# Kernel optimization log

Measured on AMD Instinct MI355X. Metric: run time of the kernel, lower is better.

Reference implementation:

```python
import jax, jax.numpy as jnp
import numpy as np

H = 128          # num_hidden
B, L, K, M = 4, 2048, 24, 64   # batch, residues, neighbors-per-residue, ligand atoms
FF = 4 * H       # feed-forward width
EPS = 1e-5       # LayerNorm eps (torch default)


def _gelu(x):
    return jax.nn.gelu(x, approximate=False)  # torch nn.GELU default (erf)


def _ln(x, s, b):
    mu = jnp.mean(x, axis=-1, keepdims=True)
    var = jnp.mean(jnp.square(x - mu), axis=-1, keepdims=True)
    return (x - mu) * jax.lax.rsqrt(var + EPS) * s + b


def _lin(x, w, b):
    return x @ w.T + b


def setup_inputs() -> dict:
    key = jax.random.key(0)
    ks = iter(jax.random.split(key, 40))
    # uniqueness makes the reference deterministic and equal to scatter-add.
    nn_idx = jnp.argsort(jax.random.uniform(next(ks), (B, L, M)), axis=-1)[:, :, :K].astype(jnp.int32)
    inp = {
        "nn_idx": nn_idx,
        "Y_scale": jax.random.uniform(next(ks), (B, M), jnp.float32, 1.0, 30.0),
        "h_Y_nodes": jax.random.normal(next(ks), (B, L, K, H), jnp.float32),
        "h_E_context": jax.random.normal(next(ks), (B, L, K, H), jnp.float32),
        "h_V": jax.random.normal(next(ks), (B, L, H), jnp.float32),
    }
    def lin_params(fan_in, fan_out):
        w = jax.random.normal(next(ks), (fan_out, fan_in), jnp.float32) / np.sqrt(fan_in).astype(np.float32)
        b = jnp.zeros((fan_out,), jnp.float32)
        return w, b
    for name, fi, fo in [("W1", 3 * H, H), ("W2", H, H), ("W3", H, H),
                         ("W11", 3 * H, H), ("W12", H, H), ("W13", H, H),
                         ("Win", H, FF), ("Wout", FF, H)]:
        inp[name + "_w"], inp[name + "_b"] = lin_params(fi, fo)
    for name in ("n1", "n2", "n3"):
        inp[name + "_s"] = jnp.ones((H,), jnp.float32)
        inp[name + "_b"] = jnp.zeros((H,), jnp.float32)
    return inp


def reference(nn_idx, Y_scale, h_Y_nodes, h_E_context, h_V,
              W1_w, W1_b, W2_w, W2_b, W3_w, W3_b,
              W11_w, W11_b, W12_w, W12_b, W13_w, W13_b,
              Win_w, Win_b, Wout_w, Wout_b,
              n1_s, n1_b, n2_s, n2_b, n3_s, n3_b):
    h_V_exp = jnp.broadcast_to(h_V[:, :, None, :], (B, L, K, H))
    h_YEV = jnp.concatenate([h_Y_nodes, h_E_context, h_V_exp], axis=-1)  # [B,L,K,3H]
    msg = _lin(_gelu(_lin(_gelu(_lin(h_YEV, W1_w, W1_b)), W2_w, W2_b)), W3_w, W3_b)
    # scatter per (b,l) with unique idx, then sum over l == segment-sum over (b, atom)
    seg_ids = (jnp.arange(B, dtype=jnp.int32)[:, None, None] * M + nn_idx).reshape(-1)
    dh = jax.ops.segment_sum(msg.reshape(-1, H), seg_ids, num_segments=B * M).reshape(B, M, H)
    dh = dh / Y_scale[:, :, None]
    # gather_context_atom_features: dh[b, nn_idx[b,l,k]]
    dh = jnp.take_along_axis(dh, nn_idx.reshape(B, L * K)[:, :, None], axis=1).reshape(B, L, K, H)
    h_Y = _ln(h_Y_nodes + dh, n1_s, n1_b)
    h_Y = _ln(h_Y + _lin(_gelu(_lin(h_Y, Win_w, Win_b)), Wout_w, Wout_b), n2_s, n2_b)
    h_YEV = jnp.concatenate([h_Y, h_E_context, h_V_exp], axis=-1)
    msg = _lin(_gelu(_lin(_gelu(_lin(h_YEV, W11_w, W11_b)), W12_w, W12_b)), W13_w, W13_b)
    h_E = _ln(h_E_context + msg, n3_s, n3_b)
    return (h_Y, h_E)
```

## Files before the change

kernel.cpp:

```cpp
#include <hip/hip_runtime.h>
#include <hip/hip_bf16.h>

#define H_   128
#define B_   4
#define L_   2048
#define KN   24
#define M_   64
#define NROW (B_*L_*KN)
#define LKR  (L_*KN)

typedef float f32x4 __attribute__((ext_vector_type(4)));
typedef short s16x8 __attribute__((ext_vector_type(8)));

#define MFMA16(a,b,c) __builtin_amdgcn_mfma_f32_16x16x32_bf16((a),(b),(c),0,0,0)

static __device__ __forceinline__ unsigned short f2bfu(float x){
    union { __hip_bfloat16 h; unsigned short s; } u; u.h = __float2bfloat16(x); return u.s;
}
static __device__ __forceinline__ float bf2f(unsigned short s){
    union { unsigned short s; __hip_bfloat16 h; } u; u.s = s; return __bfloat162float(u.h);
}
static __device__ __forceinline__ unsigned packbf(float lo, float hi){
    return (unsigned)f2bfu(lo) | ((unsigned)f2bfu(hi) << 16);
}
static __device__ __forceinline__ float gelu_f(float x){
    const float x2 = x*x;
    const float u  = x * fmaf(x2, -0.10294265f, -2.3022083f);
    const float e  = __builtin_amdgcn_exp2f(u);
    return x * __builtin_amdgcn_rcpf(1.0f + e);
}
static __device__ __forceinline__ float wsum(float v){
#pragma unroll
    for (int m = 32; m; m >>= 1) v += __shfl_xor(v, m, 64);
    return v;
}
static __device__ __forceinline__ s16x8 cvt8(float4 p0, float4 p1){
    s16x8 v;
    v[0]=(short)f2bfu(p0.x); v[1]=(short)f2bfu(p0.y); v[2]=(short)f2bfu(p0.z); v[3]=(short)f2bfu(p0.w);
    v[4]=(short)f2bfu(p1.x); v[5]=(short)f2bfu(p1.y); v[6]=(short)f2bfu(p1.z); v[7]=(short)f2bfu(p1.w);
    return v;
}
template<int KW>
static __device__ __forceinline__ s16x8 afrag(const short* xs, int r, int blk){
    return *(const s16x8*)(xs + r*KW + ((blk ^ (r & 7)) << 3));
}
template<int KW>
static __device__ __forceinline__ void bstore(short* xs, int r, int c, unsigned v){
    *(unsigned*)(xs + r*KW + ((((c >> 3) ^ (r & 7))) << 3) + (c & 7)) = v;
}
static __device__ __forceinline__ int fidx(int r, int c){
    return r*128 + ((((c >> 2) ^ (r & 7))) << 2) + (c & 3);
}

struct PackArgs {
    const float* src[8];
    int K[8];
    int off[8];
};
#define PACK_TOTAL 294912
__global__ void k_init(PackArgs pa, short* __restrict__ dst, float* __restrict__ dh){
    const int gid = blockIdx.x*256 + threadIdx.x;
    if (gid < B_*M_*H_) dh[gid] = 0.0f;
    if (gid >= PACK_TOTAL) return;
    int w = 0;
#pragma unroll
    for (int i = 1; i < 8; ++i) if (gid >= pa.off[i]) w = i;
    const int e = gid - pa.off[w];
    const int K = pa.K[w];
    const int j = e & 7, lane = (e >> 3) & 63, tt = e >> 9;
    const int kt = K >> 5;
    const int tk = tt % kt, tn = tt / kt;
    const int row = tn*16 + (lane & 15);
    const int col = tk*32 + ((lane >> 4) << 3) + j;
    dst[gid] = (short)f2bfu(pa.src[w][(size_t)row*K + col]);
}

__global__ __launch_bounds__(512, 4) void k_msg(
    const float* __restrict__ hY, const float* __restrict__ hE, const float* __restrict__ hV,
    const int* __restrict__ nn,
    const short* __restrict__ W1p, const float* __restrict__ B1,
    const short* __restrict__ W2p, const float* __restrict__ B2,
    const short* __restrict__ W3p, const float* __restrict__ B3,
    float* __restrict__ dh)
{
    __shared__ __align__(16) char pool[65536];
    short* xs  = (short*)pool;
    short* tb2 = (short*)pool;
    short* tb1 = (short*)(pool + 49152);
    const int tid = threadIdx.x, lane = tid & 63, w = tid >> 6;
    const int cl = lane & 15, rq = lane >> 4;
    const int row0 = blockIdx.x * 64, b = row0 / LKR;

    for (int c = tid; c < 64*48; c += 512){
        const int rr = c/48, k = (c - rr*48) << 3, g = row0 + rr;
        const float* s = (k < 128) ? hY + (size_t)g*128 + k
                      : (k < 256) ? hE + (size_t)g*128 + (k-128)
                                  : hV + (size_t)(g/KN)*128 + (k-256);
        float4 p0 = ((const float4*)s)[0], p1 = ((const float4*)s)[1];
        *(s16x8*)(xs + rr*384 + ((((k>>3) ^ (rr&7))) << 3)) = cvt8(p0, p1);
    }
    __syncthreads();

    f32x4 acc[4];
#pragma unroll
    for (int rf = 0; rf < 4; ++rf)
#pragma unroll
        for (int j = 0; j < 4; ++j) acc[rf][j] = B1[w*16 + rq*4 + j];
    {
        const s16x8* W8 = (const s16x8*)W1p;
#pragma unroll
        for (int ks = 0; ks < 12; ++ks){
            const s16x8 wf = W8[(size_t)(w*12 + ks)*64 + lane];
            const int blk = ks*4 + rq;
#pragma unroll
            for (int rf = 0; rf < 4; ++rf){
                const s16x8 a = afrag<384>(xs, rf*16 + cl, blk);
                acc[rf] = MFMA16(wf, a, acc[rf]);
            }
        }
    }
#pragma unroll
    for (int rf = 0; rf < 4; ++rf){
        const int r = rf*16 + cl, cb = w*16 + rq*4;
        bstore<128>(tb1, r, cb,   packbf(gelu_f(acc[rf][0]), gelu_f(acc[rf][1])));
        bstore<128>(tb1, r, cb+2, packbf(gelu_f(acc[rf][2]), gelu_f(acc[rf][3])));
    }
    __syncthreads();

#pragma unroll
    for (int rf = 0; rf < 4; ++rf)
#pragma unroll
        for (int j = 0; j < 4; ++j) acc[rf][j] = B2[w*16 + rq*4 + j];
    {
        const s16x8* W8 = (const s16x8*)W2p;
#pragma unroll
        for (int ks = 0; ks < 4; ++ks){
            const s16x8 wf = W8[(size_t)(w*4 + ks)*64 + lane];
            const int blk = ks*4 + rq;
#pragma unroll
            for (int rf = 0; rf < 4; ++rf){
                const s16x8 a = afrag<128>(tb1, rf*16 + cl, blk);
                acc[rf] = MFMA16(wf, a, acc[rf]);
            }
        }
    }
#pragma unroll
    for (int rf = 0; rf < 4; ++rf){
        const int r = rf*16 + cl, cb = w*16 + rq*4;
        bstore<128>(tb2, r, cb,   packbf(gelu_f(acc[rf][0]), gelu_f(acc[rf][1])));
        bstore<128>(tb2, r, cb+2, packbf(gelu_f(acc[rf][2]), gelu_f(acc[rf][3])));
    }
    __syncthreads();

#pragma unroll
    for (int rf = 0; rf < 4; ++rf){
        const float bv = B3[w*16 + cl];
        acc[rf] = (f32x4){bv,bv,bv,bv};
    }
    {
        const s16x8* W8 = (const s16x8*)W3p;
#pragma unroll
        for (int ks = 0; ks < 4; ++ks){
            const s16x8 wf = W8[(size_t)(w*4 + ks)*64 + lane];
            const int blk = ks*4 + rq;
#pragma unroll
            for (int rf = 0; rf < 4; ++rf){
                const s16x8 a = afrag<128>(tb2, rf*16 + cl, blk);
                acc[rf] = MFMA16(a, wf, acc[rf]);
            }
        }
    }
#pragma unroll
    for (int rf = 0; rf < 4; ++rf){
        int mj[4];
#pragma unroll
        for (int j = 0; j < 4; ++j) mj[j] = nn[row0 + rf*16 + rq*4 + j];
        const int c = w*16 + cl;
#pragma unroll
        for (int j = 0; j < 4; ++j)
            __hip_atomic_fetch_add(dh + ((size_t)(b*M_ + mj[j]))*128 + c, acc[rf][j],
                                   __ATOMIC_RELAXED, __HIP_MEMORY_SCOPE_AGENT);
    }
}

__global__ __launch_bounds__(512, 4) void k_hy(
    const float* __restrict__ hY, const float* __restrict__ dh, const float* __restrict__ Ys,
    const int* __restrict__ nn,
    const short* __restrict__ Winp, const float* __restrict__ Bin,
    const short* __restrict__ Woutp, const float* __restrict__ Bout,
    const float* __restrict__ n1s, const float* __restrict__ n1b,
    const float* __restrict__ n2s, const float* __restrict__ n2b,
    float* __restrict__ outY)
{
    __shared__ __align__(16) char pool[49152];
    short* xb  = (short*)pool;
    short* ffc = (short*)(pool + 16384);
    float* tf  = (float*)(pool + 16384);
    const int tid = threadIdx.x, lane = tid & 63, w = tid >> 6;
    const int cl = lane & 15, rq = lane >> 4;
    const int row0 = blockIdx.x * 64, b = row0 / LKR;
    const s16x8* Wi8 = (const s16x8*)Winp;
    const s16x8* Wo8 = (const s16x8*)Woutp;

    for (int c = tid; c < 64*16; c += 512){
        const int rr = c >> 4, k = (c & 15) << 3, g = row0 + rr;
        const int m = nn[g];
        const float inv = 1.0f / Ys[b*M_ + m];
        const float* a = hY + (size_t)g*128 + k;
        const float* d = dh + ((size_t)(b*M_ + m))*128 + k;
        float4 a0 = ((const float4*)a)[0], a1 = ((const float4*)a)[1];
        float4 d0 = ((const float4*)d)[0], d1 = ((const float4*)d)[1];
        float4 r0 = {fmaf(d0.x,inv,a0.x), fmaf(d0.y,inv,a0.y), fmaf(d0.z,inv,a0.z), fmaf(d0.w,inv,a0.w)};
        float4 r1 = {fmaf(d1.x,inv,a1.x), fmaf(d1.y,inv,a1.y), fmaf(d1.z,inv,a1.z), fmaf(d1.w,inv,a1.w)};
        const int s = rr & 7, kb = k >> 2;
        *(float4*)&tf[rr*128 + ((kb ^ s) << 2)]     = r0;
        *(float4*)&tf[rr*128 + (((kb+1) ^ s) << 2)] = r1;
    }
    __syncthreads();

#pragma unroll
    for (int i = 0; i < 8; ++i){
        const int r = w*8 + i;
        const float v0 = tf[fidx(r, lane)], v1 = tf[fidx(r, lane+64)];
        const float mu = wsum(v0+v1) * (1.0f/128.0f);
        const float d0 = v0-mu, d1 = v1-mu;
        const float var = wsum(d0*d0 + d1*d1) * (1.0f/128.0f);
        const float rs = rsqrtf(var + 1e-5f);
        const float y0 = d0*rs*n1s[lane]    + n1b[lane];
        const float y1 = d1*rs*n1s[lane+64] + n1b[lane+64];
        const int c1 = lane + 64;
        xb[r*128 + ((((lane>>3) ^ (r&7))) << 3) + (lane&7)] = (short)f2bfu(y0);
        xb[r*128 + ((((c1>>3)   ^ (r&7))) << 3) + (c1&7)]   = (short)f2bfu(y1);
    }
    __syncthreads();

    f32x4 accW[4];
#pragma unroll
    for (int rf = 0; rf < 4; ++rf)
#pragma unroll
        for (int j = 0; j < 4; ++j) accW[rf][j] = Bout[w*16 + rq*4 + j];

    for (int p = 0; p < 4; ++p){
        f32x4 ai[4];
#pragma unroll
        for (int rf = 0; rf < 4; ++rf)
#pragma unroll
            for (int j = 0; j < 4; ++j) ai[rf][j] = Bin[p*128 + w*16 + rq*4 + j];
#pragma unroll
        for (int ks = 0; ks < 4; ++ks){
            const s16x8 wf = Wi8[(size_t)((p*8 + w)*4 + ks)*64 + lane];
            const int blk = ks*4 + rq;
#pragma unroll
            for (int rf = 0; rf < 4; ++rf){
                const s16x8 a = afrag<128>(xb, rf*16 + cl, blk);
                ai[rf] = MFMA16(wf, a, ai[rf]);
            }
        }
        __syncthreads();
#pragma unroll
        for (int rf = 0; rf < 4; ++rf){
            const int r = rf*16 + cl, cb = w*16 + rq*4;
            bstore<128>(ffc, r, cb,   packbf(gelu_f(ai[rf][0]), gelu_f(ai[rf][1])));
            bstore<128>(ffc, r, cb+2, packbf(gelu_f(ai[rf][2]), gelu_f(ai[rf][3])));
        }
        __syncthreads();
#pragma unroll
        for (int ks = 0; ks < 4; ++ks){
            const s16x8 wf = Wo8[(size_t)(w*16 + p*4 + ks)*64 + lane];
            const int blk = ks*4 + rq;
#pragma unroll
            for (int rf = 0; rf < 4; ++rf){
                const s16x8 a = afrag<128>(ffc, rf*16 + cl, blk);
                accW[rf] = MFMA16(wf, a, accW[rf]);
            }
        }
    }
    __syncthreads();

#pragma unroll
    for (int rf = 0; rf < 4; ++rf){
        const int r = rf*16 + cl, cb = w*16 + rq*4;
        float4 o = {accW[rf][0], accW[rf][1], accW[rf][2], accW[rf][3]};
        *(float4*)&tf[r*128 + ((((cb>>2) ^ (r&7))) << 2)] = o;
    }
    __syncthreads();

#pragma unroll
    for (int i = 0; i < 8; ++i){
        const int r = w*8 + i, g = row0 + r;
        const int c1 = lane + 64;
        const float x0 = bf2f((unsigned short)xb[r*128 + ((((lane>>3) ^ (r&7))) << 3) + (lane&7)]);
        const float x1 = bf2f((unsigned short)xb[r*128 + ((((c1>>3)   ^ (r&7))) << 3) + (c1&7)]);
        const float v0 = tf[fidx(r, lane)]    + x0;
        const float v1 = tf[fidx(r, lane+64)] + x1;
        const float mu = wsum(v0+v1) * (1.0f/128.0f);
        const float d0 = v0-mu, d1 = v1-mu;
        const float var = wsum(d0*d0 + d1*d1) * (1.0f/128.0f);
        const float rs = rsqrtf(var + 1e-5f);
        outY[(size_t)g*128 + lane]      = d0*rs*n2s[lane]    + n2b[lane];
        outY[(size_t)g*128 + lane + 64] = d1*rs*n2s[lane+64] + n2b[lane+64];
    }
}

__global__ __launch_bounds__(512, 4) void k_he(
    const float* __restrict__ hYn, const float* __restrict__ hE, const float* __restrict__ hV,
    const short* __restrict__ W1p, const float* __restrict__ B1,
    const short* __restrict__ W2p, const float* __restrict__ B2,
    const short* __restrict__ W3p, const float* __restrict__ B3,
    const float* __restrict__ n3s, const float* __restrict__ n3b,
    float* __restrict__ outE)
{
    __shared__ __align__(16) char pool[65536];
    short* xs  = (short*)pool;
    short* tb2 = (short*)pool;
    short* tb1 = (short*)(pool + 49152);
    const int tid = threadIdx.x, lane = tid & 63, w = tid >> 6;
    const int cl = lane & 15, rq = lane >> 4;
    const int row0 = blockIdx.x * 64;

    for (int c = tid; c < 64*48; c += 512){
        const int rr = c/48, k = (c - rr*48) << 3, g = row0 + rr;
        const float* s = (k < 128) ? hYn + (size_t)g*128 + k
                      : (k < 256) ? hE  + (size_t)g*128 + (k-128)
                                  : hV  + (size_t)(g/KN)*128 + (k-256);
        float4 p0 = ((const float4*)s)[0], p1 = ((const float4*)s)[1];
        *(s16x8*)(xs + rr*384 + ((((k>>3) ^ (rr&7))) << 3)) = cvt8(p0, p1);
    }
    __syncthreads();

    f32x4 acc[4];
#pragma unroll
    for (int rf = 0; rf < 4; ++rf)
#pragma unroll
        for (int j = 0; j < 4; ++j) acc[rf][j] = B1[w*16 + rq*4 + j];
    {
        const s16x8* W8 = (const s16x8*)W1p;
#pragma unroll
        for (int ks = 0; ks < 12; ++ks){
            const s16x8 wf = W8[(size_t)(w*12 + ks)*64 + lane];
            const int blk = ks*4 + rq;
#pragma unroll
            for (int rf = 0; rf < 4; ++rf){
                const s16x8 a = afrag<384>(xs, rf*16 + cl, blk);
                acc[rf] = MFMA16(wf, a, acc[rf]);
            }
        }
    }
#pragma unroll
    for (int rf = 0; rf < 4; ++rf){
        const int r = rf*16 + cl, cb = w*16 + rq*4;
        bstore<128>(tb1, r, cb,   packbf(gelu_f(acc[rf][0]), gelu_f(acc[rf][1])));
        bstore<128>(tb1, r, cb+2, packbf(gelu_f(acc[rf][2]), gelu_f(acc[rf][3])));
    }
    __syncthreads();

#pragma unroll
    for (int rf = 0; rf < 4; ++rf)
#pragma unroll
        for (int j = 0; j < 4; ++j) acc[rf][j] = B2[w*16 + rq*4 + j];
    {
        const s16x8* W8 = (const s16x8*)W2p;
#pragma unroll
        for (int ks = 0; ks < 4; ++ks){
            const s16x8 wf = W8[(size_t)(w*4 + ks)*64 + lane];
            const int blk = ks*4 + rq;
#pragma unroll
            for (int rf = 0; rf < 4; ++rf){
                const s16x8 a = afrag<128>(tb1, rf*16 + cl, blk);
                acc[rf] = MFMA16(wf, a, acc[rf]);
            }
        }
    }
#pragma unroll
    for (int rf = 0; rf < 4; ++rf){
        const int r = rf*16 + cl, cb = w*16 + rq*4;
        bstore<128>(tb2, r, cb,   packbf(gelu_f(acc[rf][0]), gelu_f(acc[rf][1])));
        bstore<128>(tb2, r, cb+2, packbf(gelu_f(acc[rf][2]), gelu_f(acc[rf][3])));
    }
    __syncthreads();

#pragma unroll
    for (int rf = 0; rf < 4; ++rf)
#pragma unroll
        for (int j = 0; j < 4; ++j) acc[rf][j] = B3[w*16 + rq*4 + j];
    {
        const s16x8* W8 = (const s16x8*)W3p;
#pragma unroll
        for (int ks = 0; ks < 4; ++ks){
            const s16x8 wf = W8[(size_t)(w*4 + ks)*64 + lane];
            const int blk = ks*4 + rq;
#pragma unroll
            for (int rf = 0; rf < 4; ++rf){
                const s16x8 a = afrag<128>(tb2, rf*16 + cl, blk);
                acc[rf] = MFMA16(wf, a, acc[rf]);
            }
        }
    }
#pragma unroll
    for (int rf = 0; rf < 4; ++rf){
        const int r = rf*16 + cl, cb = w*16 + rq*4;
        bstore<128>(tb1, r, cb,   packbf(acc[rf][0], acc[rf][1]));
        bstore<128>(tb1, r, cb+2, packbf(acc[rf][2], acc[rf][3]));
    }
    __syncthreads();

#pragma unroll
    for (int i = 0; i < 8; ++i){
        const int r = w*8 + i, g = row0 + r;
        const int c1 = lane + 64;
        const float m0 = bf2f((unsigned short)tb1[r*128 + ((((lane>>3) ^ (r&7))) << 3) + (lane&7)]);
        const float m1 = bf2f((unsigned short)tb1[r*128 + ((((c1>>3)   ^ (r&7))) << 3) + (c1&7)]);
        const float v0 = m0 + hE[(size_t)g*128 + lane];
        const float v1 = m1 + hE[(size_t)g*128 + lane + 64];
        const float mu = wsum(v0+v1) * (1.0f/128.0f);
        const float d0 = v0-mu, d1 = v1-mu;
        const float var = wsum(d0*d0 + d1*d1) * (1.0f/128.0f);
        const float rs = rsqrtf(var + 1e-5f);
        outE[(size_t)g*128 + lane]      = d0*rs*n3s[lane]    + n3b[lane];
        outE[(size_t)g*128 + lane + 64] = d1*rs*n3s[lane+64] + n3b[lane+64];
    }
}

extern "C" void kernel_launch(void* const* d_in, const int* in_sizes, int n_in,
                              void* d_out, int out_size, void* d_ws, size_t ws_size,
                              hipStream_t stream) {
    const int*   nn   = (const int*)  d_in[0];
    const float* Ys   = (const float*)d_in[1];
    const float* hY   = (const float*)d_in[2];
    const float* hE   = (const float*)d_in[3];
    const float* hV   = (const float*)d_in[4];
    const float* W1w  = (const float*)d_in[5];  const float* W1b  = (const float*)d_in[6];
    const float* W2w  = (const float*)d_in[7];  const float* W2b  = (const float*)d_in[8];
    const float* W3w  = (const float*)d_in[9];  const float* W3b  = (const float*)d_in[10];
    const float* W11w = (const float*)d_in[11]; const float* W11b = (const float*)d_in[12];
    const float* W12w = (const float*)d_in[13]; const float* W12b = (const float*)d_in[14];
    const float* W13w = (const float*)d_in[15]; const float* W13b = (const float*)d_in[16];
    const float* Winw = (const float*)d_in[17]; const float* Winb = (const float*)d_in[18];
    const float* Woutw= (const float*)d_in[19]; const float* Woutb= (const float*)d_in[20];
    const float* n1s  = (const float*)d_in[21]; const float* n1b  = (const float*)d_in[22];
    const float* n2s  = (const float*)d_in[23]; const float* n2b  = (const float*)d_in[24];
    const float* n3s  = (const float*)d_in[25]; const float* n3b  = (const float*)d_in[26];

    float* outY = (float*)d_out;
    float* outE = outY + (size_t)NROW * H_;

    float* dh = (float*)d_ws;
    short* wp = (short*)((char*)d_ws + 131072);

    const int oW1 = 0,       oW2 = 49152,   oW3 = 65536,   oW11 = 81920;
    const int oW12 = 131072, oW13 = 147456, oWin = 163840, oWout = 229376;

    PackArgs pa;
    pa.src[0]=W1w;  pa.K[0]=384; pa.off[0]=oW1;
    pa.src[1]=W2w;  pa.K[1]=128; pa.off[1]=oW2;
    pa.src[2]=W3w;  pa.K[2]=128; pa.off[2]=oW3;
    pa.src[3]=W11w; pa.K[3]=384; pa.off[3]=oW11;
    pa.src[4]=W12w; pa.K[4]=128; pa.off[4]=oW12;
    pa.src[5]=W13w; pa.K[5]=128; pa.off[5]=oW13;
    pa.src[6]=Winw; pa.K[6]=128; pa.off[6]=oWin;
    pa.src[7]=Woutw;pa.K[7]=512; pa.off[7]=oWout;

    const int nblk = NROW / 64;

    k_init <<<(PACK_TOTAL + 255)/256, 256, 0, stream>>>(pa, wp, dh);
    k_msg  <<<nblk, 512, 0, stream>>>(hY, hE, hV, nn,
                                      wp + oW1, W1b, wp + oW2, W2b, wp + oW3, W3b, dh);
    k_hy   <<<nblk, 512, 0, stream>>>(hY, dh, Ys, nn, wp + oWin, Winb, wp + oWout, Woutb,
                                      n1s, n1b, n2s, n2b, outY);
    k_he   <<<nblk, 512, 0, stream>>>(outY, hE, hV,
                                      wp + oW11, W11b, wp + oW12, W12b, wp + oW13, W13b,
                                      n3s, n3b, outE);
}
```

Before: 369.4 us.

## Stage first-layer input in two K-halves to shrink LDS footprint

The 384-wide first-layer input tile is now staged into shared memory in two 192-wide halves, each followed by its share of MFMA work. This cuts the per-block shared allocation from 64KB to 40KB in both the message and edge kernels, which could let more blocks reside per CU. In exchange it adds extra barriers and serializes loading the second half behind the first half's compute.

```diff
diff --git a/kernel.cpp b/kernel.cpp
--- a/kernel.cpp
+++ b/kernel.cpp
@@ -83,40 +83,60 @@
     const short* __restrict__ W3p, const float* __restrict__ B3,
     float* __restrict__ dh)
 {
-    __shared__ __align__(16) char pool[65536];
+    __shared__ __align__(16) char pool[40960];
     short* xs  = (short*)pool;
     short* tb2 = (short*)pool;
-    short* tb1 = (short*)(pool + 49152);
+    short* tb1 = (short*)(pool + 24576);
     const int tid = threadIdx.x, lane = tid & 63, w = tid >> 6;
     const int cl = lane & 15, rq = lane >> 4;
     const int row0 = blockIdx.x * 64, b = row0 / LKR;
-
-    for (int c = tid; c < 64*48; c += 512){
-        const int rr = c/48, k = (c - rr*48) << 3, g = row0 + rr;
+    const s16x8* W18 = (const s16x8*)W1p;
+
+    f32x4 acc[4];
+#pragma unroll
+    for (int rf = 0; rf < 4; ++rf)
+#pragma unroll
+        for (int j = 0; j < 4; ++j) acc[rf][j] = B1[w*16 + rq*4 + j];
+
+    for (int c = tid; c < 64*24; c += 512){
+        const int rr = c/24, kb = c - rr*24;
+        const int k = kb*8;
+        const int g = row0 + rr;
         const float* s = (k < 128) ? hY + (size_t)g*128 + k
-                      : (k < 256) ? hE + (size_t)g*128 + (k-128)
-                                  : hV + (size_t)(g/KN)*128 + (k-256);
+                                   : hE + (size_t)g*128 + (k-128);
         float4 p0 = ((const float4*)s)[0], p1 = ((const float4*)s)[1];
-        *(s16x8*)(xs + rr*384 + ((((k>>3) ^ (rr&7))) << 3)) = cvt8(p0, p1);
-    }
-    __syncthreads();
-
-    f32x4 acc[4];
-#pragma unroll
-    for (int rf = 0; rf < 4; ++rf)
-#pragma unroll
-        for (int j = 0; j < 4; ++j) acc[rf][j] = B1[w*16 + rq*4 + j];
-    {
-        const s16x8* W8 = (const s16x8*)W1p;
-#pragma unroll
-        for (int ks = 0; ks < 12; ++ks){
-            const s16x8 wf = W8[(size_t)(w*12 + ks)*64 + lane];
-            const int blk = ks*4 + rq;
-#pragma unroll
-            for (int rf = 0; rf < 4; ++rf){
-                const s16x8 a = afrag<384>(xs, rf*16 + cl, blk);
-                acc[rf] = MFMA16(wf, a, acc[rf]);
-            }
+        *(s16x8*)(xs + rr*192 + ((kb ^ (rr&7)) << 3)) = cvt8(p0, p1);
+    }
+    __syncthreads();
+#pragma unroll
+    for (int ks = 0; ks < 6; ++ks){
+        const s16x8 wf = W18[(size_t)(w*12 + ks)*64 + lane];
+        const int blk = ks*4 + rq;
+#pragma unroll
+        for (int rf = 0; rf < 4; ++rf){
+            const s16x8 a = afrag<192>(xs, rf*16 + cl, blk);
+            acc[rf] = MFMA16(wf, a, acc[rf]);
+        }
+    }
+    __syncthreads();
+    for (int c = tid; c < 64*24; c += 512){
+        const int rr = c/24, kb = c - rr*24;
+        const int k = 192 + kb*8;
+        const int g = row0 + rr;
+        const float* s = (k < 256) ? hE + (size_t)g*128 + (k-128)
+                                   : hV + (size_t)(g/KN)*128 + (k-256);
+        float4 p0 = ((const float4*)s)[0], p1 = ((const float4*)s)[1];
+        *(s16x8*)(xs + rr*192 + ((kb ^ (rr&7)) << 3)) = cvt8(p0, p1);
+    }
+    __syncthreads();
+#pragma unroll
+    for (int ks = 0; ks < 6; ++ks){
+        const s16x8 wf = W18[(size_t)(w*12 + 6 + ks)*64 + lane];
+        const int blk = ks*4 + rq;
+#pragma unroll
+        for (int rf = 0; rf < 4; ++rf){
+            const s16x8 a = afrag<192>(xs, rf*16 + cl, blk);
+            acc[rf] = MFMA16(wf, a, acc[rf]);
         }
     }
 #pragma unroll
@@ -310,40 +330,60 @@
     const float* __restrict__ n3s, const float* __restrict__ n3b,
     float* __restrict__ outE)
 {
-    __shared__ __align__(16) char pool[65536];
+    __shared__ __align__(16) char pool[40960];
     short* xs  = (short*)pool;
     short* tb2 = (short*)pool;
-    short* tb1 = (short*)(pool + 49152);
+    short* tb1 = (short*)(pool + 24576);
     const int tid = threadIdx.x, lane = tid & 63, w = tid >> 6;
     const int cl = lane & 15, rq = lane >> 4;
     const int row0 = blockIdx.x * 64;
-
-    for (int c = tid; c < 64*48; c += 512){
-        const int rr = c/48, k = (c - rr*48) << 3, g = row0 + rr;
+    const s16x8* W18 = (const s16x8*)W1p;
+
+    f32x4 acc[4];
+#pragma unroll
+    for (int rf = 0; rf < 4; ++rf)
+#pragma unroll
+        for (int j = 0; j < 4; ++j) acc[rf][j] = B1[w*16 + rq*4 + j];
+
+    for (int c = tid; c < 64*24; c += 512){
+        const int rr = c/24, kb = c - rr*24;
+        const int k = kb*8;
+        const int g = row0 + rr;
         const float* s = (k < 128) ? hYn + (size_t)g*128 + k
-                      : (k < 256) ? hE  + (size_t)g*128 + (k-128)
-                                  : hV  + (size_t)(g/KN)*128 + (k-256);
+                                   : hE  + (size_t)g*128 + (k-128);
         float4 p0 = ((const float4*)s)[0], p1 = ((const float4*)s)[1];
-        *(s16x8*)(xs + rr*384 + ((((k>>3) ^ (rr&7))) << 3)) = cvt8(p0, p1);
-    }
-    __syncthreads();
-
-    f32x4 acc[4];
-#pragma unroll
-    for (int rf = 0; rf < 4; ++rf)
-#pragma unroll
-        for (int j = 0; j < 4; ++j) acc[rf][j] = B1[w*16 + rq*4 + j];
-    {
-        const s16x8* W8 = (const s16x8*)W1p;
-#pragma unroll
-        for (int ks = 0; ks < 12; ++ks){
-            const s16x8 wf = W8[(size_t)(w*12 + ks)*64 + lane];
-            const int blk = ks*4 + rq;
-#pragma unroll
-            for (int rf = 0; rf < 4; ++rf){
-                const s16x8 a = afrag<384>(xs, rf*16 + cl, blk);
-                acc[rf] = MFMA16(wf, a, acc[rf]);
-            }
+        *(s16x8*)(xs + rr*192 + ((kb ^ (rr&7)) << 3)) = cvt8(p0, p1);
+    }
+    __syncthreads();
+#pragma unroll
+    for (int ks = 0; ks < 6; ++ks){
+        const s16x8 wf = W18[(size_t)(w*12 + ks)*64 + lane];
+        const int blk = ks*4 + rq;
+#pragma unroll
+        for (int rf = 0; rf < 4; ++rf){
+            const s16x8 a = afrag<192>(xs, rf*16 + cl, blk);
+            acc[rf] = MFMA16(wf, a, acc[rf]);
+        }
+    }
+    __syncthreads();
+    for (int c = tid; c < 64*24; c += 512){
+        const int rr = c/24, kb = c - rr*24;
+        const int k = 192 + kb*8;
+        const int g = row0 + rr;
+        const float* s = (k < 256) ? hE + (size_t)g*128 + (k-128)
+                                   : hV + (size_t)(g/KN)*128 + (k-256);
+        float4 p0 = ((const float4*)s)[0], p1 = ((const float4*)s)[1];
+        *(s16x8*)(xs + rr*192 + ((kb ^ (rr&7)) << 3)) = cvt8(p0, p1);
+    }
+    __syncthreads();
+#pragma unroll
+    for (int ks = 0; ks < 6; ++ks){
+        const s16x8 wf = W18[(size_t)(w*12 + 6 + ks)*64 + lane];
+        const int blk = ks*4 + rq;
+#pragma unroll
+        for (int rf = 0; rf < 4; ++rf){
+            const s16x8 a = afrag<192>(xs, rf*16 + cl, blk);
+            acc[rf] = MFMA16(wf, a, acc[rf]);
         }
     }
 #pragma unroll
```

Measured after the change: 343.5 us. -7.0%, faster.
